# Kernel optimization log

Hardware: AMD Instinct MI355X
Metric: run time of the kernel (lower is better)

Reference implementation:

```python
import jax, jax.numpy as jnp
import numpy as np

B, N, DIN, DOUT, RATIO, K = 8, 4096, 128, 256, 4, 16
S = N // RATIO
BN_EPS = 1e-5


def furthest_point_sample(xyz, n_samples):
    # xyz: [B, N, 3] -> idx [B, n_samples] int32. Sequential farthest-distance reduction.
    b, n, _ = xyz.shape
    dist0 = jnp.full((b, n), 1e10, xyz.dtype)
    last0 = xyz[:, 0, :]  # first sampled point is index 0 (CUDA kernel convention)

    def step(carry, _):
        dist, last = carry
        d = jnp.sum((xyz - last[:, None, :]) ** 2, axis=-1)  # [B, N]
        dist = jnp.minimum(dist, d)
        nxt = jnp.argmax(dist, axis=1).astype(jnp.int32)      # [B]
        last = jnp.take_along_axis(xyz, nxt[:, None, None].astype(jnp.int32), axis=1)[:, 0, :]
        return (dist, last), nxt

    (_, _), idxs = jax.lax.scan(step, (dist0, last0), None, length=n_samples - 1)
    idx = jnp.concatenate([jnp.zeros((1, b), jnp.int32), idxs], axis=0).T  # [B, S]
    return idx


def knn_indices(query, points, k):
    # query [B,S,3], points [B,N,3] -> k nearest indices [B,S,k]
    q2 = jnp.sum(query ** 2, axis=-1)                           # [B,S]
    p2 = jnp.sum(points ** 2, axis=-1)                          # [B,N]
    d2 = q2[:, :, None] + p2[:, None, :] - 2.0 * jnp.einsum('bsd,bnd->bsn', query, points)
    _, idx = jax.lax.top_k(-d2, k)                              # smallest distances
    return idx


def setup_inputs() -> dict:
    key = jax.random.key(0)
    k1, k2, k3, k4 = jax.random.split(key, 4)
    input_feature = jax.random.normal(k1, (B, N, DIN), dtype=jnp.float32)
    xyz = jax.random.uniform(k2, (B, N, 3), dtype=jnp.float32)
    # linear params (torch nn.Linear: W [out,in], b [out])
    lim = 1.0 / np.sqrt(DIN)
    W = jax.random.uniform(k3, (DOUT, DIN), dtype=jnp.float32, minval=-lim, maxval=lim)
    b = jax.random.uniform(k4, (DOUT,), dtype=jnp.float32, minval=-lim, maxval=lim)
    gamma = jnp.ones((DOUT,), jnp.float32)
    beta = jnp.zeros((DOUT,), jnp.float32)
    return {"input_feature": input_feature, "xyz": xyz, "W": W, "b": b, "gamma": gamma, "beta": beta}


def reference(input_feature, xyz, W, b, gamma, beta):
    sample_idx = furthest_point_sample(xyz, S)                         # [B,S]
    sample_xyz = jnp.take_along_axis(xyz, sample_idx[:, :, None], axis=1)  # [B,S,3]
    knn_idx = knn_indices(sample_xyz, xyz, K)                          # [B,S,K]
    # gather_knn: [B,S,K,DIN]
    knn_feat = jax.vmap(lambda f, i: f[i])(input_feature, knn_idx)
    h = jnp.einsum('bskd,ed->bske', knn_feat, W) + b                   # linear [B,S,K,DOUT]
    # BatchNorm1d over channel dim, stats across (B, S*K) in training mode (biased var)
    mean = jnp.mean(h, axis=(0, 1, 2))
    var = jnp.var(h, axis=(0, 1, 2))
    h = gamma * (h - mean) * jax.lax.rsqrt(var + BN_EPS) + beta
    h = jax.nn.relu(h)
    sample_feature = jnp.max(h, axis=2)                                # [B,S,DOUT]
    return sample_feature, sample_xyz
```

## Files before the change

### kernel.cpp

```cpp
#include <hip/hip_runtime.h>
#include <hip/hip_bf16.h>

#define BB 8
#define NN 4096
#define DIN 128
#define DOUT 256
#define SS 1024
#define KK 16

__device__ float g_g[(size_t)BB * NN * DOUT];
__device__ int   g_knn[BB * SS * KK];
__device__ int   g_wcount[BB * NN];
__device__ float g_S1[DOUT];
__device__ float g_S2[DOUT];

__device__ __forceinline__ unsigned long long umax64(unsigned long long a, unsigned long long b) {
    return a > b ? a : b;
}

__global__ __launch_bounds__(512) void k_fused1(
    const float* __restrict__ feat, const float* __restrict__ xyz,
    const float* __restrict__ W, const float* __restrict__ bias,
    float* __restrict__ out)
{
    __shared__ __align__(16) float smem[16384];
    __shared__ __align__(16) unsigned long long swk64[2][8];

    if (blockIdx.x < BB) {
        #pragma clang fp contract(off)
        const int b = blockIdx.x, tid = threadIdx.x;
        const float* bx = xyz + (size_t)b * NN * 3;
        for (int i = 0; i < 8; ++i) {
            int p = tid + i * 512;
            float4 v; v.x = bx[p*3]; v.y = bx[p*3+1]; v.z = bx[p*3+2]; v.w = 0.f;
            ((float4*)smem)[p] = v;
        }
        __syncthreads();
        float px[8], py[8], pz[8];
        double dist64[8];
        unsigned fb[8];
        unsigned long long key[8];
        const int gbase = tid * 8;
        const unsigned long long D0 =
            ((unsigned long long)__double_as_longlong(1e10)) & ~0xFFFULL;
        #pragma unroll
        for (int r = 0; r < 8; ++r) {
            float4 v = ((float4*)smem)[gbase + r];
            px[r] = v.x; py[r] = v.y; pz[r] = v.z;
            dist64[r] = 1e10;
            fb[r] = __float_as_uint(1e10f);
            key[r] = D0 | (unsigned long long)(4095 - (gbase + r));
        }
        float4 c0 = ((float4*)smem)[0];
        float lxf = c0.x, lyf = c0.y, lzf = c0.z;
        double lxd = (double)lxf, lyd = (double)lyf, lzd = (double)lzf;
        float* oxyz = out + (size_t)BB * SS * DOUT;
        if (tid == 0) {
            oxyz[(size_t)(b*SS)*3]   = lxf;
            oxyz[(size_t)(b*SS)*3+1] = lyf;
            oxyz[(size_t)(b*SS)*3+2] = lzf;
        }
        for (int s = 1; s < SS; ++s) {
            #pragma unroll
            for (int r = 0; r < 8; ++r) {
                float dx = px[r] - lxf, dy = py[r] - lyf, dz = pz[r] - lzf;
                float d32 = fmaf(dx, dx, fmaf(dy, dy, dz * dz));
                unsigned du = __float_as_uint(d32);
                if (du < fb[r] + 16u) {
                    double ddx = (double)px[r] - lxd;
                    double ddy = (double)py[r] - lyd;
                    double ddz = (double)pz[r] - lzd;
                    double m1 = ddx*ddx, m2 = ddy*ddy, m3 = ddz*ddz;
                    double d = (m1 + m2) + m3;
                    if (d < dist64[r]) {
                        dist64[r] = d;
                        fb[r] = __float_as_uint((float)d);
                        key[r] = (((unsigned long long)__double_as_longlong(d)) & ~0xFFFULL)
                                 | (unsigned long long)(4095 - (gbase + r));
                    }
                }
            }
            unsigned long long kk;
            {
                unsigned long long a0 = umax64(key[0], key[1]);
                unsigned long long a1 = umax64(key[2], key[3]);
                unsigned long long a2 = umax64(key[4], key[5]);
                unsigned long long a3 = umax64(key[6], key[7]);
                kk = umax64(umax64(a0, a1), umax64(a2, a3));
            }
#define DPP64(CTRL) { \
    int _lo = __builtin_amdgcn_update_dpp(0, (int)(unsigned)kk, CTRL, 0xf, 0xf, true); \
    int _hi = __builtin_amdgcn_update_dpp(0, (int)(unsigned)(kk >> 32), CTRL, 0xf, 0xf, true); \
    unsigned long long _o = (((unsigned long long)(unsigned)_hi) << 32) | (unsigned)_lo; \
    if (_o > kk) kk = _o; }
            DPP64(0x111)
            DPP64(0x112)
            DPP64(0x114)
            DPP64(0x118)
            DPP64(0x142)
            DPP64(0x143)
#undef DPP64
            if ((tid & 63) == 63) swk64[s & 1][tid >> 6] = kk;
            __syncthreads();
            const unsigned long long* sw = swk64[s & 1];
            unsigned long long k01 = umax64(sw[0], sw[1]);
            unsigned long long k23 = umax64(sw[2], sw[3]);
            unsigned long long k45 = umax64(sw[4], sw[5]);
            unsigned long long k67 = umax64(sw[6], sw[7]);
            unsigned long long kmax = umax64(umax64(k01, k23), umax64(k45, k67));
            int widx = 4095 - (int)(kmax & 0xFFFULL);
            float4 c = ((float4*)smem)[widx];
            lxf = c.x; lyf = c.y; lzf = c.z;
            lxd = (double)c.x; lyd = (double)c.y; lzd = (double)c.z;
            if (tid == 0) {
                oxyz[(size_t)(b*SS+s)*3]   = c.x;
                oxyz[(size_t)(b*SS+s)*3+1] = c.y;
                oxyz[(size_t)(b*SS+s)*3+2] = c.z;
            }
        }
    } else if (blockIdx.x < BB + 2048) {
        int gi = blockIdx.x - BB;
        int mt = gi & 511, nt = gi >> 9;
        int rbase = mt * 64, cbase = nt * 64;
        float* As = smem;
        float* Bs = smem + 64 * 36;
        int tid = threadIdx.x;
        int tx = tid & 15, ty = tid >> 4;
        int c0 = tx * 4, r0 = ty * 2;
        int lr = tid >> 3;
        int lk = (tid & 7) * 4;
        float acc[2][4] = {{0.f,0.f,0.f,0.f},{0.f,0.f,0.f,0.f}};
        for (int kc = 0; kc < 4; ++kc) {
            __syncthreads();
            float4 av = *(const float4*)&feat[(size_t)(rbase + lr) * DIN + kc*32 + lk];
            *(float4*)&As[lr * 36 + lk] = av;
            float4 wv = *(const float4*)&W[(size_t)(cbase + lr) * DIN + kc*32 + lk];
            Bs[(lk+0)*68 + lr] = wv.x;
            Bs[(lk+1)*68 + lr] = wv.y;
            Bs[(lk+2)*68 + lr] = wv.z;
            Bs[(lk+3)*68 + lr] = wv.w;
            __syncthreads();
            const float* Ar0 = &As[r0 * 36];
            const float* Ar1 = Ar0 + 36;
            #pragma unroll
            for (int k = 0; k < 32; ++k) {
                float a0 = Ar0[k], a1 = Ar1[k];
                float4 bv = *(float4*)&Bs[k * 68 + c0];
                acc[0][0] += a0 * bv.x; acc[0][1] += a0 * bv.y;
                acc[0][2] += a0 * bv.z; acc[0][3] += a0 * bv.w;
                acc[1][0] += a1 * bv.x; acc[1][1] += a1 * bv.y;
                acc[1][2] += a1 * bv.z; acc[1][3] += a1 * bv.w;
            }
        }
        float4 bb4 = *(const float4*)&bias[cbase + c0];
        float4 o0, o1;
        o0.x = acc[0][0] + bb4.x; o0.y = acc[0][1] + bb4.y;
        o0.z = acc[0][2] + bb4.z; o0.w = acc[0][3] + bb4.w;
        o1.x = acc[1][0] + bb4.x; o1.y = acc[1][1] + bb4.y;
        o1.z = acc[1][2] + bb4.z; o1.w = acc[1][3] + bb4.w;
        *(float4*)&g_g[(size_t)(rbase + r0)     * DOUT + cbase + c0] = o0;
        *(float4*)&g_g[(size_t)(rbase + r0 + 1) * DOUT + cbase + c0] = o1;
    } else {
        int zi = blockIdx.x - (BB + 2048);
        int t = zi * 512 + threadIdx.x;
        g_wcount[t] = 0;
        g_wcount[t + 16384] = 0;
        if (t < DOUT) { g_S1[t] = 0.f; g_S2[t] = 0.f; }
    }
}

__global__ __launch_bounds__(1024) void k_knn(
    const float* __restrict__ xyz, const float* __restrict__ out)
{
    __shared__ __align__(16) float4 pts[NN];
    __shared__ unsigned hist[16][512];
    __shared__ int cand[16][128];
    __shared__ int cnt[16];
    const int tid = threadIdx.x, lane = tid & 63, w = tid >> 6;
    const int q = blockIdx.x * 16 + w;
    const int b = blockIdx.x >> 6;
    const float* bx = xyz + (size_t)b * NN * 3;
    for (int i = 0; i < 4; ++i) {
        int p = tid + i * 1024;
        float4 v; v.x = bx[p*3]; v.y = bx[p*3+1]; v.z = bx[p*3+2]; v.w = 0.f;
        pts[p] = v;
    }
    { unsigned* h = &hist[0][0];
      #pragma unroll
      for (int i = 0; i < 8; ++i) h[tid + i * 1024] = 0u; }
    if (tid < 16) cnt[tid] = 0;
    __syncthreads();

    const float* sx = out + (size_t)BB * SS * DOUT + (size_t)q * 3;
    const float qxf = sx[0], qyf = sx[1], qzf = sx[2];
    unsigned minub = 0xFFFFFFFFu;
    for (int t = 0; t < 64; ++t) {
        int n = t * 64 + lane;
        float4 p = pts[n];
        float dx = qxf - p.x, dy = qyf - p.y, dz = qzf - p.z;
        float df = fmaf(dz, dz, fmaf(dy, dy, dx * dx));
        unsigned ub = __float_as_uint(df);
        minub = ub < minub ? ub : minub;
        unsigned bk = ub < 0x30800000u ? 0u : ((ub - 0x30800000u) >> 19);
        bk = bk > 511u ? 511u : bk;
        atomicAdd(&hist[w][bk], 1u);
    }
    #pragma unroll
    for (int m = 1; m < 64; m <<= 1) {
        unsigned o = __shfl_xor(minub, m);
        minub = o < minub ? o : minub;
    }
    unsigned mb = minub < 0x30800000u ? 0u : ((minub - 0x30800000u) >> 19);
    mb = mb > 511u ? 511u : mb;
    int Tb = 511;
    unsigned base = 0;
    for (int ch = (int)(mb >> 6); ch < 8; ++ch) {
        unsigned v = hist[w][ch * 64 + lane];
        #pragma unroll
        for (int m = 1; m < 64; m <<= 1) {
            unsigned t2 = __shfl_up(v, m);
            if (lane >= m) v += t2;
        }
        unsigned tot = __shfl(v, 63);
        unsigned long long msk = __ballot(base + v >= 16u);
        if (msk) { Tb = ch * 64 + (__ffsll(msk) - 1); break; }
        base += tot;
    }
    unsigned Tcap = (unsigned)Tb + 1u; Tcap = Tcap > 511u ? 511u : Tcap;
    for (int t = 0; t < 64; ++t) {
        int n = t * 64 + lane;
        float4 p = pts[n];
        float dx = qxf - p.x, dy = qyf - p.y, dz = qzf - p.z;
        float df = fmaf(dz, dz, fmaf(dy, dy, dx * dx));
        unsigned ub = __float_as_uint(df);
        unsigned bk = ub < 0x30800000u ? 0u : ((ub - 0x30800000u) >> 19);
        bk = bk > 511u ? 511u : bk;
        if (bk <= Tcap) {
            int slot = atomicAdd(&cnt[w], 1);
            if (slot < 128) cand[w][slot] = n;
        }
    }
    {
        #pragma clang fp contract(off)
        int count = cnt[w]; count = count > 128 ? 128 : count;
        const double qx = (double)qxf, qy = (double)qyf, qz = (double)qzf;
        int i0 = lane < count ? cand[w][lane] : -1;
        int i1 = (lane + 64) < count ? cand[w][lane + 64] : -1;
        double d0 = 1e300, d1 = 1e300;
        if (i0 >= 0) {
            float4 p = pts[i0];
            double dx = qx - (double)p.x, dy = qy - (double)p.y, dz = qz - (double)p.z;
            double m1 = dx*dx, m2 = dy*dy, m3 = dz*dz;
            d0 = (m1 + m2) + m3;
        }
        if (i1 >= 0) {
            float4 p = pts[i1];
            double dx = qx - (double)p.x, dy = qy - (double)p.y, dz = qz - (double)p.z;
            double m1 = dx*dx, m2 = dy*dy, m3 = dz*dz;
            d1 = (m1 + m2) + m3;
        }
        int r0 = 0, r1 = 0;
        for (int i = 0; i < count; ++i) {
            double od; int oi;
            if (i < 64) { od = __shfl(d0, i);      oi = __shfl(i0, i); }
            else        { od = __shfl(d1, i - 64); oi = __shfl(i1, i - 64); }
            if ((od < d0) || (od == d0 && oi < i0)) ++r0;
            if ((od < d1) || (od == d1 && oi < i1)) ++r1;
        }
        if (i0 >= 0 && r0 < KK) {
            g_knn[(size_t)q * KK + r0] = i0;
            atomicAdd(&g_wcount[b * NN + i0], 1);
        }
        if (i1 >= 0 && r1 < KK) {
            g_knn[(size_t)q * KK + r1] = i1;
            atomicAdd(&g_wcount[b * NN + i1], 1);
        }
    }
}

__global__ __launch_bounds__(256) void k_stats()
{
    int tid = threadIdx.x;
    int rbase = blockIdx.x * 128;
    float a1 = 0.f, a2 = 0.f;
    for (int i = 0; i < 128; ++i) {
        int row = rbase + i;
        int w = g_wcount[row];
        if (w) {
            float v = g_g[(size_t)row * DOUT + tid];
            float wf = (float)w;
            a1 += wf * v;
            a2 += wf * v * v;
        }
    }
    atomicAdd(&g_S1[tid], a1);
    atomicAdd(&g_S2[tid], a2);
}

__global__ __launch_bounds__(256) void k_final(
    const float* __restrict__ gamma, const float* __restrict__ beta,
    float* __restrict__ out)
{
    int w = threadIdx.x >> 6, lane = threadIdx.x & 63;
    int q = blockIdx.x * 4 + w;
    int b = q >> 10;
    int c = lane * 4;
    const int* ki = g_knn + (size_t)q * KK;
    float4 m; m.x = m.y = m.z = m.w = -1e30f;
    for (int k = 0; k < KK; ++k) {
        int idx = ki[k];
        float4 v = *(const float4*)&g_g[((size_t)(b * NN + idx)) * DOUT + c];
        m.x = fmaxf(m.x, v.x); m.y = fmaxf(m.y, v.y);
        m.z = fmaxf(m.z, v.z); m.w = fmaxf(m.w, v.w);
    }
    const float inv = 1.0f / 131072.0f;
    float4 s1 = *(const float4*)&g_S1[c];
    float4 s2 = *(const float4*)&g_S2[c];
    float4 ga = *(const float4*)&gamma[c];
    float4 be = *(const float4*)&beta[c];
    float4 o;
    {
        float mean = s1.x * inv; float var = s2.x * inv - mean * mean;
        float rs = rsqrtf(var + 1e-5f);
        float t = ga.x * (m.x - mean); t = t * rs; t += be.x; o.x = fmaxf(t, 0.f);
    }
    {
        float mean = s1.y * inv; float var = s2.y * inv - mean * mean;
        float rs = rsqrtf(var + 1e-5f);
        float t = ga.y * (m.y - mean); t = t * rs; t += be.y; o.y = fmaxf(t, 0.f);
    }
    {
        float mean = s1.z * inv; float var = s2.z * inv - mean * mean;
        float rs = rsqrtf(var + 1e-5f);
        float t = ga.z * (m.z - mean); t = t * rs; t += be.z; o.z = fmaxf(t, 0.f);
    }
    {
        float mean = s1.w * inv; float var = s2.w * inv - mean * mean;
        float rs = rsqrtf(var + 1e-5f);
        float t = ga.w * (m.w - mean); t = t * rs; t += be.w; o.w = fmaxf(t, 0.f);
    }
    *(float4*)&out[(size_t)q * DOUT + c] = o;
}

extern "C" void kernel_launch(void* const* d_in, const int* in_sizes, int n_in,
                              void* d_out, int out_size, void* d_ws, size_t ws_size,
                              hipStream_t stream) {
    (void)in_sizes; (void)n_in; (void)out_size; (void)d_ws; (void)ws_size;
    const float* feat  = (const float*)d_in[0];
    const float* xyz   = (const float*)d_in[1];
    const float* W     = (const float*)d_in[2];
    const float* bias  = (const float*)d_in[3];
    const float* gamma = (const float*)d_in[4];
    const float* beta  = (const float*)d_in[5];
    float* out = (float*)d_out;

    k_fused1<<<BB + 2048 + 32, 512, 0, stream>>>(feat, xyz, W, bias, out);
    k_knn   <<<BB * SS / 16, 1024, 0, stream>>>(xyz, out);
    k_stats <<<256, 256, 0, stream>>>();
    k_final <<<2048, 256, 0, stream>>>(gamma, beta, out);
}
```

Measured before the change: 1.021 ms.

## Halve FPS block width, pack distance math with v_pk ops, widen GEMM tiles

The fused first kernel drops from 512 to 256 threads per block. The farthest-point-sampling block now holds 16 points per thread and computes the float32 screening distance two points at a time with packed v_pk_add/mul/fma instructions. The cross-wave reduction shrinks from 8 to 4 wave partials, and the refine threshold is stored as a precomputed float. The GEMM blocks keep the same 64x64 tile but each thread computes a 4x4 micro-tile, and the zeroing blocks clear four entries per thread. The goal is to shorten the serial FPS critical path, which costs one barrier per sample, and to raise register reuse in the GEMM, at the cost of more registers per thread and fewer threads per block.

After: 1.329 ms. +30.2%, slower.

```diff
diff --git a/kernel.cpp b/kernel.cpp
--- a/kernel.cpp
+++ b/kernel.cpp
@@ -14,46 +14,61 @@
 __device__ float g_S1[DOUT];
 __device__ float g_S2[DOUT];
 
+typedef float f32x2 __attribute__((ext_vector_type(2)));
+
 __device__ __forceinline__ unsigned long long umax64(unsigned long long a, unsigned long long b) {
     return a > b ? a : b;
 }
-
-__global__ __launch_bounds__(512) void k_fused1(
+__device__ __forceinline__ f32x2 pk_add(f32x2 a, f32x2 b) {
+    f32x2 d; asm("v_pk_add_f32 %0, %1, %2" : "=v"(d) : "v"(a), "v"(b)); return d;
+}
+__device__ __forceinline__ f32x2 pk_mul(f32x2 a, f32x2 b) {
+    f32x2 d; asm("v_pk_mul_f32 %0, %1, %2" : "=v"(d) : "v"(a), "v"(b)); return d;
+}
+__device__ __forceinline__ f32x2 pk_fma(f32x2 a, f32x2 b, f32x2 c) {
+    f32x2 d; asm("v_pk_fma_f32 %0, %1, %2, %3" : "=v"(d) : "v"(a), "v"(b), "v"(c)); return d;
+}
+
+__global__ __launch_bounds__(256) void k_fused1(
     const float* __restrict__ feat, const float* __restrict__ xyz,
     const float* __restrict__ W, const float* __restrict__ bias,
     float* __restrict__ out)
 {
     __shared__ __align__(16) float smem[16384];
-    __shared__ __align__(16) unsigned long long swk64[2][8];
+    __shared__ __align__(16) unsigned long long swk64[2][4];
 
     if (blockIdx.x < BB) {
         #pragma clang fp contract(off)
         const int b = blockIdx.x, tid = threadIdx.x;
         const float* bx = xyz + (size_t)b * NN * 3;
-        for (int i = 0; i < 8; ++i) {
-            int p = tid + i * 512;
+        for (int i = 0; i < 16; ++i) {
+            int p = tid + i * 256;
             float4 v; v.x = bx[p*3]; v.y = bx[p*3+1]; v.z = bx[p*3+2]; v.w = 0.f;
             ((float4*)smem)[p] = v;
         }
         __syncthreads();
-        float px[8], py[8], pz[8];
-        double dist64[8];
-        unsigned fb[8];
-        unsigned long long key[8];
-        const int gbase = tid * 8;
+        f32x2 px2[8], py2[8], pz2[8];
+        double dist64[16];
+        float thr[16];
+        unsigned long long key[16];
+        const int gbase = tid * 16;
         const unsigned long long D0 =
             ((unsigned long long)__double_as_longlong(1e10)) & ~0xFFFULL;
+        const float THR0 = __uint_as_float(__float_as_uint(1e10f) + 16u);
         #pragma unroll
-        for (int r = 0; r < 8; ++r) {
-            float4 v = ((float4*)smem)[gbase + r];
-            px[r] = v.x; py[r] = v.y; pz[r] = v.z;
-            dist64[r] = 1e10;
-            fb[r] = __float_as_uint(1e10f);
-            key[r] = D0 | (unsigned long long)(4095 - (gbase + r));
-        }
-        float4 c0 = ((float4*)smem)[0];
-        float lxf = c0.x, lyf = c0.y, lzf = c0.z;
-        double lxd = (double)lxf, lyd = (double)lyf, lzd = (double)lzf;
+        for (int pp = 0; pp < 8; ++pp) {
+            float4 v0 = ((float4*)smem)[gbase + 2*pp];
+            float4 v1 = ((float4*)smem)[gbase + 2*pp + 1];
+            px2[pp].x = v0.x; px2[pp].y = v1.x;
+            py2[pp].x = v0.y; py2[pp].y = v1.y;
+            pz2[pp].x = v0.z; pz2[pp].y = v1.z;
+            dist64[2*pp]   = 1e10; dist64[2*pp+1] = 1e10;
+            thr[2*pp] = THR0;      thr[2*pp+1] = THR0;
+            key[2*pp]   = D0 | (unsigned long long)(4095 - (gbase + 2*pp));
+            key[2*pp+1] = D0 | (unsigned long long)(4095 - (gbase + 2*pp + 1));
+        }
+        float4 c0v = ((float4*)smem)[0];
+        float lxf = c0v.x, lyf = c0v.y, lzf = c0v.z;
         float* oxyz = out + (size_t)BB * SS * DOUT;
         if (tid == 0) {
             oxyz[(size_t)(b*SS)*3]   = lxf;
@@ -61,20 +76,42 @@
             oxyz[(size_t)(b*SS)*3+2] = lzf;
         }
         for (int s = 1; s < SS; ++s) {
+            const double lxd = (double)lxf, lyd = (double)lyf, lzd = (double)lzf;
+            f32x2 nlx; nlx.x = -lxf; nlx.y = -lxf;
+            f32x2 nly; nly.x = -lyf; nly.y = -lyf;
+            f32x2 nlz; nlz.x = -lzf; nlz.y = -lzf;
             #pragma unroll
-            for (int r = 0; r < 8; ++r) {
-                float dx = px[r] - lxf, dy = py[r] - lyf, dz = pz[r] - lzf;
-                float d32 = fmaf(dx, dx, fmaf(dy, dy, dz * dz));
-                unsigned du = __float_as_uint(d32);
-                if (du < fb[r] + 16u) {
-                    double ddx = (double)px[r] - lxd;
-                    double ddy = (double)py[r] - lyd;
-                    double ddz = (double)pz[r] - lzd;
+            for (int pp = 0; pp < 8; ++pp) {
+                f32x2 dx = pk_add(px2[pp], nlx);
+                f32x2 dy = pk_add(py2[pp], nly);
+                f32x2 dz = pk_add(pz2[pp], nlz);
+                f32x2 d2 = pk_mul(dx, dx);
+                d2 = pk_fma(dy, dy, d2);
+                d2 = pk_fma(dz, dz, d2);
+                if (d2.x < thr[2*pp]) {
+                    const int r = 2*pp;
+                    double ddx = (double)px2[pp].x - lxd;
+                    double ddy = (double)py2[pp].x - lyd;
+                    double ddz = (double)pz2[pp].x - lzd;
                     double m1 = ddx*ddx, m2 = ddy*ddy, m3 = ddz*ddz;
                     double d = (m1 + m2) + m3;
                     if (d < dist64[r]) {
                         dist64[r] = d;
-                        fb[r] = __float_as_uint((float)d);
+                        thr[r] = __uint_as_float(__float_as_uint((float)d) + 16u);
+                        key[r] = (((unsigned long long)__double_as_longlong(d)) & ~0xFFFULL)
+                                 | (unsigned long long)(4095 - (gbase + r));
+                    }
+                }
+                if (d2.y < thr[2*pp+1]) {
+                    const int r = 2*pp + 1;
+                    double ddx = (double)px2[pp].y - lxd;
+                    double ddy = (double)py2[pp].y - lyd;
+                    double ddz = (double)pz2[pp].y - lzd;
+                    double m1 = ddx*ddx, m2 = ddy*ddy, m3 = ddz*ddz;
+                    double d = (m1 + m2) + m3;
+                    if (d < dist64[r]) {
+                        dist64[r] = d;
+                        thr[r] = __uint_as_float(__float_as_uint((float)d) + 16u);
                         key[r] = (((unsigned long long)__double_as_longlong(d)) & ~0xFFFULL)
                                  | (unsigned long long)(4095 - (gbase + r));
                     }
@@ -86,7 +123,15 @@
                 unsigned long long a1 = umax64(key[2], key[3]);
                 unsigned long long a2 = umax64(key[4], key[5]);
                 unsigned long long a3 = umax64(key[6], key[7]);
-                kk = umax64(umax64(a0, a1), umax64(a2, a3));
+                unsigned long long a4 = umax64(key[8], key[9]);
+                unsigned long long a5 = umax64(key[10], key[11]);
+                unsigned long long a6 = umax64(key[12], key[13]);
+                unsigned long long a7 = umax64(key[14], key[15]);
+                unsigned long long b0 = umax64(a0, a1);
+                unsigned long long b1 = umax64(a2, a3);
+                unsigned long long b2 = umax64(a4, a5);
+                unsigned long long b3 = umax64(a6, a7);
+                kk = umax64(umax64(b0, b1), umax64(b2, b3));
             }
 #define DPP64(CTRL) { \
     int _lo = __builtin_amdgcn_update_dpp(0, (int)(unsigned)kk, CTRL, 0xf, 0xf, true); \
@@ -103,15 +148,10 @@
             if ((tid & 63) == 63) swk64[s & 1][tid >> 6] = kk;
             __syncthreads();
             const unsigned long long* sw = swk64[s & 1];
-            unsigned long long k01 = umax64(sw[0], sw[1]);
-            unsigned long long k23 = umax64(sw[2], sw[3]);
-            unsigned long long k45 = umax64(sw[4], sw[5]);
-            unsigned long long k67 = umax64(sw[6], sw[7]);
-            unsigned long long kmax = umax64(umax64(k01, k23), umax64(k45, k67));
+            unsigned long long kmax = umax64(umax64(sw[0], sw[1]), umax64(sw[2], sw[3]));
             int widx = 4095 - (int)(kmax & 0xFFFULL);
             float4 c = ((float4*)smem)[widx];
             lxf = c.x; lyf = c.y; lzf = c.z;
-            lxd = (double)c.x; lyd = (double)c.y; lzd = (double)c.z;
             if (tid == 0) {
                 oxyz[(size_t)(b*SS+s)*3]   = c.x;
                 oxyz[(size_t)(b*SS+s)*3+1] = c.y;
@@ -126,45 +166,61 @@
         float* Bs = smem + 64 * 36;
         int tid = threadIdx.x;
         int tx = tid & 15, ty = tid >> 4;
-        int c0 = tx * 4, r0 = ty * 2;
-        int lr = tid >> 3;
-        int lk = (tid & 7) * 4;
-        float acc[2][4] = {{0.f,0.f,0.f,0.f},{0.f,0.f,0.f,0.f}};
+        int c0 = tx * 4, r0 = ty * 4;
+        int lr = tid >> 2;
+        int lk = (tid & 3) * 8;
+        float acc[4][4] = {{0.f,0.f,0.f,0.f},{0.f,0.f,0.f,0.f},
+                           {0.f,0.f,0.f,0.f},{0.f,0.f,0.f,0.f}};
         for (int kc = 0; kc < 4; ++kc) {
             __syncthreads();
-            float4 av = *(const float4*)&feat[(size_t)(rbase + lr) * DIN + kc*32 + lk];
-            *(float4*)&As[lr * 36 + lk] = av;
-            float4 wv = *(const float4*)&W[(size_t)(cbase + lr) * DIN + kc*32 + lk];
-            Bs[(lk+0)*68 + lr] = wv.x;
-            Bs[(lk+1)*68 + lr] = wv.y;
-            Bs[(lk+2)*68 + lr] = wv.z;
-            Bs[(lk+3)*68 + lr] = wv.w;
+            float4 a0 = *(const float4*)&feat[(size_t)(rbase + lr) * DIN + kc*32 + lk];
+            float4 a1 = *(const float4*)&feat[(size_t)(rbase + lr) * DIN + kc*32 + lk + 4];
+            *(float4*)&As[lr * 36 + lk]     = a0;
+            *(float4*)&As[lr * 36 + lk + 4] = a1;
+            float4 w0 = *(const float4*)&W[(size_t)(cbase + lr) * DIN + kc*32 + lk];
+            float4 w1 = *(const float4*)&W[(size_t)(cbase + lr) * DIN + kc*32 + lk + 4];
+            Bs[(lk+0)*68 + lr] = w0.x;
+            Bs[(lk+1)*68 + lr] = w0.y;
+            Bs[(lk+2)*68 + lr] = w0.z;
+            Bs[(lk+3)*68 + lr] = w0.w;
+            Bs[(lk+4)*68 + lr] = w1.x;
+            Bs[(lk+5)*68 + lr] = w1.y;
+            Bs[(lk+6)*68 + lr] = w1.z;
+            Bs[(lk+7)*68 + lr] = w1.w;
             __syncthreads();
-            const float* Ar0 = &As[r0 * 36];
-            const float* Ar1 = Ar0 + 36;
+            const float* Ar0 = &As[(r0+0) * 36];
+            const float* Ar1 = &As[(r0+1) * 36];
+            const float* Ar2 = &As[(r0+2) * 36];
+            const float* Ar3 = &As[(r0+3) * 36];
             #pragma unroll
             for (int k = 0; k < 32; ++k) {
-                float a0 = Ar0[k], a1 = Ar1[k];
+                float a0v = Ar0[k], a1v = Ar1[k], a2v = Ar2[k], a3v = Ar3[k];
                 float4 bv = *(float4*)&Bs[k * 68 + c0];
-                acc[0][0] += a0 * bv.x; acc[0][1] += a0 * bv.y;
-                acc[0][2] += a0 * bv.z; acc[0][3] += a0 * bv.w;
-                acc[1][0] += a1 * bv.x; acc[1][1] += a1 * bv.y;
-                acc[1][2] += a1 * bv.z; acc[1][3] += a1 * bv.w;
+                acc[0][0] += a0v * bv.x; acc[0][1] += a0v * bv.y;
+                acc[0][2] += a0v * bv.z; acc[0][3] += a0v * bv.w;
+                acc[1][0] += a1v * bv.x; acc[1][1] += a1v * bv.y;
+                acc[1][2] += a1v * bv.z; acc[1][3] += a1v * bv.w;
+                acc[2][0] += a2v * bv.x; acc[2][1] += a2v * bv.y;
+                acc[2][2] += a2v * bv.z; acc[2][3] += a2v * bv.w;
+                acc[3][0] += a3v * bv.x; acc[3][1] += a3v * bv.y;
+                acc[3][2] += a3v * bv.z; acc[3][3] += a3v * bv.w;
             }
         }
         float4 bb4 = *(const float4*)&bias[cbase + c0];
-        float4 o0, o1;
-        o0.x = acc[0][0] + bb4.x; o0.y = acc[0][1] + bb4.y;
-        o0.z = acc[0][2] + bb4.z; o0.w = acc[0][3] + bb4.w;
-        o1.x = acc[1][0] + bb4.x; o1.y = acc[1][1] + bb4.y;
-        o1.z = acc[1][2] + bb4.z; o1.w = acc[1][3] + bb4.w;
-        *(float4*)&g_g[(size_t)(rbase + r0)     * DOUT + cbase + c0] = o0;
-        *(float4*)&g_g[(size_t)(rbase + r0 + 1) * DOUT + cbase + c0] = o1;
+        #pragma unroll
+        for (int j = 0; j < 4; ++j) {
+            float4 o;
+            o.x = acc[j][0] + bb4.x; o.y = acc[j][1] + bb4.y;
+            o.z = acc[j][2] + bb4.z; o.w = acc[j][3] + bb4.w;
+            *(float4*)&g_g[(size_t)(rbase + r0 + j) * DOUT + cbase + c0] = o;
+        }
     } else {
         int zi = blockIdx.x - (BB + 2048);
-        int t = zi * 512 + threadIdx.x;
+        int t = zi * 256 + threadIdx.x;
         g_wcount[t] = 0;
+        g_wcount[t + 8192] = 0;
         g_wcount[t + 16384] = 0;
+        g_wcount[t + 24576] = 0;
         if (t < DOUT) { g_S1[t] = 0.f; g_S2[t] = 0.f; }
     }
 }
@@ -354,7 +410,7 @@
     const float* beta  = (const float*)d_in[5];
     float* out = (float*)d_out;
 
-    k_fused1<<<BB + 2048 + 32, 512, 0, stream>>>(feat, xyz, W, bias, out);
+    k_fused1<<<BB + 2048 + 32, 256, 0, stream>>>(feat, xyz, W, bias, out);
     k_knn   <<<BB * SS / 16, 1024, 0, stream>>>(xyz, out);
     k_stats <<<256, 256, 0, stream>>>();
     k_final <<<2048, 256, 0, stream>>>(gamma, beta, out);
```
